# Optimization experiments

Measured on AMD Instinct MI355X. Metric: run time of the kernel, lower is better.

The kernel has to match this reference:

```python
import jax, jax.numpy as jnp
import numpy as np
import math

EMBED = 1024
HEADS = 16
HEAD_DIM = EMBED // HEADS
FFN = 4 * EMBED
LAYERS = 3
SEQ = 2048
BATCH = 2
INPUT_DIM = 64


def make_pe(max_len, d_model):
    pe = np.zeros((max_len, d_model), dtype=np.float32)
    pos = np.arange(max_len, dtype=np.float32)[:, None]
    div = np.exp(np.arange(0, d_model, 2, dtype=np.float32) * (-math.log(10000.0) / d_model))
    pe[:, 0::2] = np.sin(pos * div)
    pe[:, 1::2] = np.cos(pos * div)
    return jnp.asarray(pe)


def setup_inputs() -> dict:
    key = jax.random.key(0)
    ks = jax.random.split(key, 16)
    s = lambda k, shape, fan: jax.random.normal(k, shape, dtype=jnp.float32) / np.sqrt(fan)
    return {
        "x": jax.random.normal(ks[0], (BATCH, SEQ, INPUT_DIM), dtype=jnp.float32),
        "mask": jnp.ones((BATCH, 1, 1, SEQ), dtype=bool),
        "embed_W": s(ks[1], (INPUT_DIM, EMBED), INPUT_DIM),
        "embed_b": jnp.zeros((EMBED,), jnp.float32),
        "pe": make_pe(SEQ, EMBED),
        "Wq": s(ks[2], (LAYERS, HEAD_DIM, HEAD_DIM), HEAD_DIM),
        "Wk": s(ks[3], (LAYERS, HEAD_DIM, HEAD_DIM), HEAD_DIM),
        "Wv": s(ks[4], (LAYERS, HEAD_DIM, HEAD_DIM), HEAD_DIM),
        "Wo": s(ks[5], (LAYERS, EMBED, EMBED), EMBED),
        "bo": jnp.zeros((LAYERS, EMBED), jnp.float32),
        "ln1_g": jnp.ones((LAYERS, EMBED), jnp.float32),
        "ln1_b": jnp.zeros((LAYERS, EMBED), jnp.float32),
        "W1": s(ks[6], (LAYERS, EMBED, FFN), EMBED),
        "b1": jnp.zeros((LAYERS, FFN), jnp.float32),
        "W2": s(ks[7], (LAYERS, FFN, EMBED), FFN),
        "b2": jnp.zeros((LAYERS, EMBED), jnp.float32),
        "ln2_g": jnp.ones((LAYERS, EMBED), jnp.float32),
        "ln2_b": jnp.zeros((LAYERS, EMBED), jnp.float32),
    }


def _layernorm(x, g, b, eps=1e-5):
    mu = jnp.mean(x, axis=-1, keepdims=True)
    var = jnp.var(x, axis=-1, keepdims=True)
    return (x - mu) * jax.lax.rsqrt(var + eps) * g + b


def reference(x, mask, embed_W, embed_b, pe, Wq, Wk, Wv, Wo, bo,
              ln1_g, ln1_b, W1, b1, W2, b2, ln2_g, ln2_b):
    N, S, _ = x.shape
    scale = 1.0 / np.sqrt(EMBED).astype(np.float32)  # note: sqrt(embed_size), as in original
    h = x @ embed_W + embed_b + pe[None, :S, :]
    for l in range(LAYERS):
        hr = h.reshape(N, S, HEADS, HEAD_DIM)
        q = jnp.einsum('nshd,de->nshe', hr, Wq[l])
        k = jnp.einsum('nshd,de->nshe', hr, Wk[l])
        v = jnp.einsum('nshd,de->nshe', hr, Wv[l])
        energy = jnp.einsum('nqhd,nkhd->nhqk', q, k)  # (N,H,S,S)
        energy = jnp.where(mask == 0, jnp.float32(-1e20), energy)
        attn = jax.nn.softmax(energy * scale, axis=-1)
        o = jnp.einsum('nhqk,nkhd->nqhd', attn, v).reshape(N, S, EMBED)
        o = o @ Wo[l] + bo[l]
        x1 = _layernorm(o + h, ln1_g[l], ln1_b[l])
        ff = jax.nn.relu(x1 @ W1[l] + b1[l]) @ W2[l] + b2[l]
        h = _layernorm(ff + x1, ln2_g[l], ln2_b[l])
    return h
```

## Files before the change

### kernel.cpp

```cpp
#include <hip/hip_runtime.h>


typedef __attribute__((ext_vector_type(8))) unsigned short us8;
typedef __attribute__((ext_vector_type(4))) unsigned short us4;
typedef __attribute__((ext_vector_type(8))) __bf16 bf16x8;
typedef __attribute__((ext_vector_type(4))) float f32x4;

#define SEQ   2048
#define HEADS 16
#define HD    64
#define EMB   1024
#define FFN_  4096
#define NBAT  2
#define ROWS  (NBAT*SEQ)

__device__ __forceinline__ float bf2f(unsigned short s) {
    return __builtin_bit_cast(float, ((unsigned int)s) << 16);
}
__device__ __forceinline__ unsigned short f2bf(float f) {
    unsigned int u = __builtin_bit_cast(unsigned int, f);
    u += 0x7fffu + ((u >> 16) & 1u);
    return (unsigned short)(u >> 16);
}
__device__ __forceinline__ bf16x8 ldfrag(const unsigned short* p) {
    us8 v = *(const us8*)p;
    return __builtin_bit_cast(bf16x8, v);
}
__device__ __forceinline__ us8 cvt8(const float* p) {
    float4 f0 = *(const float4*)p, f1 = *(const float4*)(p + 4);
    us8 v;
    v[0] = f2bf(f0.x); v[1] = f2bf(f0.y); v[2] = f2bf(f0.z); v[3] = f2bf(f0.w);
    v[4] = f2bf(f1.x); v[5] = f2bf(f1.y); v[6] = f2bf(f1.z); v[7] = f2bf(f1.w);
    return v;
}
__device__ __forceinline__ void async_cp16(const unsigned short* g, unsigned short* l) {
    __builtin_amdgcn_global_load_lds(
        (const __attribute__((address_space(1))) void*)g,
        (__attribute__((address_space(3))) void*)l, 16, 0, 0);
}

__device__ __forceinline__ void transpose_tile(
    const float* __restrict__ W, unsigned short* __restrict__ Wt,
    int K, int N, int k0, int n0, int t)
{
    __shared__ float T[64][65];
    const int kk = t >> 4, nn = (t & 15) * 4;
#pragma unroll
    for (int r = 0; r < 4; r++) {
        float4 v = *(const float4*)(W + (size_t)(k0 + kk + r*16)*N + n0 + nn);
        T[kk + r*16][nn+0] = v.x; T[kk + r*16][nn+1] = v.y;
        T[kk + r*16][nn+2] = v.z; T[kk + r*16][nn+3] = v.w;
    }
    __syncthreads();
    const int n = t >> 2, kc = (t & 3) * 16;
    us8 a, b;
#pragma unroll
    for (int i = 0; i < 8; i++) a[i] = f2bf(T[kc + i][n]);
#pragma unroll
    for (int i = 0; i < 8; i++) b[i] = f2bf(T[kc + 8 + i][n]);
    *(us8*)(Wt + (size_t)(n0 + n)*K + k0 + kc)     = a;
    *(us8*)(Wt + (size_t)(n0 + n)*K + k0 + kc + 8) = b;
}

__global__ __launch_bounds__(256) void wprep(
    const float* __restrict__ W, unsigned short* __restrict__ Wt,
    const int K, const int N)
{
    transpose_tile(W, Wt, K, N, blockIdx.x*64, blockIdx.y*64, threadIdx.x);
}

__global__ __launch_bounds__(256) void wprep_qkv(
    const float* __restrict__ Wq, const float* __restrict__ Wk,
    const float* __restrict__ Wv, unsigned short* __restrict__ Wt3)
{
    const float* W = blockIdx.z == 0 ? Wq : (blockIdx.z == 1 ? Wk : Wv);
    transpose_tile(W, Wt3 + (size_t)blockIdx.z*64*64, 64, 64, 0, 0, threadIdx.x);
}

__global__ __launch_bounds__(256) void cvt_bf16(
    const float* __restrict__ src, unsigned short* __restrict__ dst, const int n8)
{
    int i = blockIdx.x*256 + threadIdx.x;
    if (i < n8) *(us8*)(dst + (size_t)i*8) = cvt8(src + (size_t)i*8);
}

__global__ __launch_bounds__(256) void vtrans(
    const unsigned short* __restrict__ QKV, unsigned short* __restrict__ Vt)
{
    __shared__ __align__(16) unsigned short T[64*72];
    const int s0 = blockIdx.x*64, h = blockIdx.y, n = blockIdx.z;
    const int t = threadIdx.x;
    const int s = t & 63, c16 = (t >> 6) * 16;
    const unsigned short* src =
        QKV + ((size_t)(n*SEQ + s0 + s)*HEADS + h)*192 + 128 + c16;
    *(us8*)&T[s*72 + c16]     = *(const us8*)(src);
    *(us8*)&T[s*72 + c16 + 8] = *(const us8*)(src + 8);
    __syncthreads();
    const int f = t & 63, r16 = (t >> 6) * 16;
    us8 a, b;
#pragma unroll
    for (int i = 0; i < 8; i++) a[i] = T[(r16 + i)*72 + f];
#pragma unroll
    for (int i = 0; i < 8; i++) b[i] = T[(r16 + 8 + i)*72 + f];
    unsigned short* dst = Vt + ((size_t)(n*HEADS + h)*HD + f)*SEQ + s0 + r16;
    *(us8*)dst       = a;
    *(us8*)(dst + 8) = b;
}

template<int BM, int BN, int WR, int WC>
__global__ __launch_bounds__(WR*WC*64) void gemm_bt(
    const unsigned short* __restrict__ A, const unsigned short* __restrict__ Bt,
    void* __restrict__ Cout, const int out_bf16,
    const float* __restrict__ bias, const float* __restrict__ pe,
    const int M, const int N, const int K, const int relu)
{
    constexpr int BK  = 32;
    constexpr int NW  = WR*WC;
    constexpr int ACH = BM*4;
    constexpr int BCH = BN*4;
    constexpr int APW = ACH/NW;
    constexpr int BPW = BCH/NW;
    __shared__ __align__(16) unsigned short As[BM*BK];
    __shared__ __align__(16) unsigned short Bs[BN*BK];

    const int tid  = threadIdx.x;
    const int lane = tid & 63;
    const int wave = tid >> 6;
    const int wm   = (wave / WC) * 64;
    const int wn   = (wave % WC) * 64;
    const int bm   = blockIdx.x * BM;
    const int bn   = blockIdx.y * BN;
    const int m15  = lane & 15;
    const int quad = lane >> 4;

    f32x4 acc[4][4];
#pragma unroll
    for (int i = 0; i < 4; i++)
#pragma unroll
        for (int j = 0; j < 4; j++) acc[i][j] = (f32x4){0.f, 0.f, 0.f, 0.f};

    for (int kt = 0; kt < K; kt += BK) {
#pragma unroll
        for (int j = 0; j < APW/64; j++) {
            const int c = wave*APW + j*64 + lane;
            async_cp16(A + (size_t)(bm + (c >> 2))*K + kt + (c & 3)*8,
                       As + (size_t)(wave*APW + j*64)*8);
        }
#pragma unroll
        for (int j = 0; j < BPW/64; j++) {
            const int c = wave*BPW + j*64 + lane;
            async_cp16(Bt + (size_t)(bn + (c >> 2))*K + kt + (c & 3)*8,
                       Bs + (size_t)(wave*BPW + j*64)*8);
        }
        __syncthreads();

        bf16x8 af[4], bfr[4];
#pragma unroll
        for (int i = 0; i < 4; i++) af[i]  = ldfrag(&As[(wm + i*16 + m15)*BK + quad*8]);
#pragma unroll
        for (int j = 0; j < 4; j++) bfr[j] = ldfrag(&Bs[(wn + j*16 + m15)*BK + quad*8]);
#pragma unroll
        for (int i = 0; i < 4; i++)
#pragma unroll
            for (int j = 0; j < 4; j++)
                acc[i][j] = __builtin_amdgcn_mfma_f32_16x16x32_bf16(af[i], bfr[j], acc[i][j], 0, 0, 0);
        __syncthreads();
    }

#pragma unroll
    for (int i = 0; i < 4; i++) {
#pragma unroll
        for (int j = 0; j < 4; j++) {
#pragma unroll
            for (int r = 0; r < 4; r++) {
                int row = bm + wm + i*16 + quad*4 + r;
                int col = bn + wn + j*16 + m15;
                float v = acc[i][j][r];
                if (bias) v += bias[col];
                if (pe)   v += pe[(size_t)(row & (SEQ-1))*EMB + col];
                if (relu) v = fmaxf(v, 0.f);
                if (out_bf16) ((unsigned short*)Cout)[(size_t)row*N + col] = f2bf(v);
                else          ((float*)Cout)[(size_t)row*N + col] = v;
            }
        }
    }
}

__global__ __launch_bounds__(256, 2) void flash_attn(
    const unsigned short* __restrict__ QKV, const unsigned short* __restrict__ Vt,
    unsigned short* __restrict__ O)
{
    const int h = blockIdx.y, n = blockIdx.z;
    const int tid = threadIdx.x, lane = tid & 63, wave = tid >> 6;
    const int m15 = lane & 15, quad = lane >> 4;
    const int q0 = blockIdx.x*128 + wave*32;

    __shared__ __align__(16) unsigned short Pl[4][32*36];

    bf16x8 aq[2][2];
#pragma unroll
    for (int mi = 0; mi < 2; mi++) {
        const unsigned short* qp =
            QKV + ((size_t)(n*SEQ + q0 + mi*16 + m15)*HEADS + h)*192;
        aq[mi][0] = ldfrag(qp + quad*8);
        aq[mi][1] = ldfrag(qp + 32 + quad*8);
    }

    f32x4 accO[2][4];
    f32x4 lacc[2];
#pragma unroll
    for (int mi = 0; mi < 2; mi++) {
        lacc[mi] = (f32x4){0.f, 0.f, 0.f, 0.f};
#pragma unroll
        for (int ft = 0; ft < 4; ft++) accO[mi][ft] = (f32x4){0.f, 0.f, 0.f, 0.f};
    }

    const float sl2e = 0.03125f * 1.4426950408889634f;
    const unsigned short* kb = QKV + ((size_t)(n*SEQ)*HEADS + h)*192 + 64;
    const unsigned short* vb = Vt + (size_t)(n*HEADS + h)*HD*SEQ;

    us8 ones_u;
#pragma unroll
    for (int i = 0; i < 8; i++) ones_u[i] = 0x3F80;
    const bf16x8 ones = __builtin_bit_cast(bf16x8, ones_u);

    auto load_kv = [&](bf16x8 (&dk)[2][2], bf16x8 (&dv)[4], int kt) {
#pragma unroll
        for (int nt = 0; nt < 2; nt++)
#pragma unroll
            for (int ks = 0; ks < 2; ks++)
                dk[nt][ks] = ldfrag(kb + (size_t)(kt + nt*16 + m15)*(HEADS*192)
                                       + ks*32 + quad*8);
#pragma unroll
        for (int ft = 0; ft < 4; ft++)
            dv[ft] = ldfrag(vb + (size_t)(ft*16 + m15)*SEQ + kt + quad*8);
    };

    auto step = [&](bf16x8 (&ck)[2][2], bf16x8 (&cv)[4],
                    bf16x8 (&nk)[2][2], bf16x8 (&nv)[4], int ktn) {
        load_kv(nk, nv, ktn);
        __builtin_amdgcn_sched_barrier(0);

        f32x4 sv[2][2];
        __builtin_amdgcn_s_setprio(1);
#pragma unroll
        for (int mi = 0; mi < 2; mi++)
#pragma unroll
            for (int nt = 0; nt < 2; nt++) {
                f32x4 z = (f32x4){0.f, 0.f, 0.f, 0.f};
                z = __builtin_amdgcn_mfma_f32_16x16x32_bf16(aq[mi][0], ck[nt][0], z, 0, 0, 0);
                z = __builtin_amdgcn_mfma_f32_16x16x32_bf16(aq[mi][1], ck[nt][1], z, 0, 0, 0);
                sv[mi][nt] = z;
            }
        __builtin_amdgcn_s_setprio(0);

#pragma unroll
        for (int mi = 0; mi < 2; mi++)
#pragma unroll
            for (int nt = 0; nt < 2; nt++)
#pragma unroll
                for (int r = 0; r < 4; r++) {
                    float p = exp2f(fminf(sv[mi][nt][r] * sl2e, 80.f));
                    Pl[wave][(mi*16 + quad*4 + r)*36 + nt*16 + m15] = f2bf(p);
                }

        bf16x8 pf[2];
#pragma unroll
        for (int mi = 0; mi < 2; mi++)
            pf[mi] = ldfrag(&Pl[wave][(mi*16 + m15)*36 + quad*8]);
        __builtin_amdgcn_s_setprio(1);
#pragma unroll
        for (int mi = 0; mi < 2; mi++) {
#pragma unroll
            for (int ft = 0; ft < 4; ft++)
                accO[mi][ft] = __builtin_amdgcn_mfma_f32_16x16x32_bf16(
                    pf[mi], cv[ft], accO[mi][ft], 0, 0, 0);
            lacc[mi] = __builtin_amdgcn_mfma_f32_16x16x32_bf16(
                pf[mi], ones, lacc[mi], 0, 0, 0);
        }
        __builtin_amdgcn_s_setprio(0);
    };

    bf16x8 k0[2][2], v0[4], k1[2][2], v1[4];
    load_kv(k0, v0, 0);
    for (int kt = 0; kt < SEQ; kt += 64) {
        step(k0, v0, k1, v1, kt + 32);
        step(k1, v1, k0, v0, (kt + 64) & (SEQ - 1));
    }

#pragma unroll
    for (int mi = 0; mi < 2; mi++)
#pragma unroll
        for (int r = 0; r < 4; r++) {
            const float inv = 1.0f / lacc[mi][r];
            const int row = q0 + mi*16 + quad*4 + r;
#pragma unroll
            for (int ft = 0; ft < 4; ft++)
                O[((size_t)(n*SEQ + row)*HEADS + h)*HD + ft*16 + m15] =
                    f2bf(accO[mi][ft][r] * inv);
        }
}

__global__ __launch_bounds__(256) void add_ln_kernel(
    const unsigned short* __restrict__ a, const unsigned short* __restrict__ res,
    const float* __restrict__ g, const float* __restrict__ b,
    void* __restrict__ out, const int out_fp32)
{
    const int row = blockIdx.x;
    const int tid = threadIdx.x;
    const int c0  = tid * 4;

    us4 va = *(const us4*)(a   + (size_t)row*EMB + c0);
    us4 vr = *(const us4*)(res + (size_t)row*EMB + c0);
    float x[4];
#pragma unroll
    for (int i = 0; i < 4; i++) x[i] = bf2f(va[i]) + bf2f(vr[i]);

    float s = x[0] + x[1] + x[2] + x[3];
    float q = x[0]*x[0] + x[1]*x[1] + x[2]*x[2] + x[3]*x[3];
#pragma unroll
    for (int off = 1; off < 64; off <<= 1) {
        s += __shfl_xor(s, off, 64);
        q += __shfl_xor(q, off, 64);
    }
    __shared__ float rs[4], rq[4];
    if ((tid & 63) == 0) { rs[tid >> 6] = s; rq[tid >> 6] = q; }
    __syncthreads();
    s = rs[0] + rs[1] + rs[2] + rs[3];
    q = rq[0] + rq[1] + rq[2] + rq[3];

    const float mu   = s * (1.0f/EMB);
    const float var  = q * (1.0f/EMB) - mu*mu;
    const float rstd = rsqrtf(var + 1e-5f);

    float4 vg = *(const float4*)(g + c0);
    float4 vb = *(const float4*)(b + c0);
    float y0 = (x[0] - mu) * rstd * vg.x + vb.x;
    float y1 = (x[1] - mu) * rstd * vg.y + vb.y;
    float y2 = (x[2] - mu) * rstd * vg.z + vb.z;
    float y3 = (x[3] - mu) * rstd * vg.w + vb.w;

    if (out_fp32) {
        *(float4*)((float*)out + (size_t)row*EMB + c0) = (float4){y0, y1, y2, y3};
    } else {
        us4 o;
        o[0] = f2bf(y0); o[1] = f2bf(y1); o[2] = f2bf(y2); o[3] = f2bf(y3);
        *(us4*)((unsigned short*)out + (size_t)row*EMB + c0) = o;
    }
}

extern "C" void kernel_launch(void* const* d_in, const int* in_sizes, int n_in,
                              void* d_out, int out_size, void* d_ws, size_t ws_size,
                              hipStream_t stream)
{
    (void)in_sizes; (void)n_in; (void)out_size; (void)ws_size;
    const float* x    = (const float*)d_in[0];
    const float* embW = (const float*)d_in[2];
    const float* embB = (const float*)d_in[3];
    const float* pe   = (const float*)d_in[4];
    const float* Wq   = (const float*)d_in[5];
    const float* Wk   = (const float*)d_in[6];
    const float* Wv   = (const float*)d_in[7];
    const float* Wo   = (const float*)d_in[8];
    const float* bo   = (const float*)d_in[9];
    const float* ln1g = (const float*)d_in[10];
    const float* ln1b = (const float*)d_in[11];
    const float* W1   = (const float*)d_in[12];
    const float* b1   = (const float*)d_in[13];
    const float* W2   = (const float*)d_in[14];
    const float* b2   = (const float*)d_in[15];
    const float* ln2g = (const float*)d_in[16];
    const float* ln2b = (const float*)d_in[17];

    char* ws = (char*)d_ws;
    const size_t MB = 1024*1024;
    unsigned short* qkv = (unsigned short*)ws;
    unsigned short* ff  = (unsigned short*)ws;
    unsigned short* vt  = (unsigned short*)(ws + 24*MB);
    unsigned short* t   = (unsigned short*)(ws + 32*MB);
    unsigned short* h   = (unsigned short*)(ws + 40*MB);
    unsigned short* x1  = (unsigned short*)(ws + 48*MB);
    unsigned short* wx  = (unsigned short*)(ws + 56*MB);
    unsigned short* xb    = t;
    unsigned short* embWt = t + 256*1024;
    unsigned short* qkvWt = t;
    unsigned short* o   = (unsigned short*)d_out;

    cvt_bf16<<<128, 256, 0, stream>>>(x, xb, ROWS*64/8);
    wprep<<<dim3(1, EMB/64), 256, 0, stream>>>(embW, embWt, 64, EMB);
    gemm_bt<128,128,2,2><<<dim3(ROWS/128, EMB/128), 256, 0, stream>>>(
        xb, embWt, h, 1, embB, pe, ROWS, EMB, 64, 0);

    for (int l = 0; l < 3; l++) {
        wprep_qkv<<<dim3(1,1,3), 256, 0, stream>>>(
            Wq + (size_t)l*HD*HD, Wk + (size_t)l*HD*HD, Wv + (size_t)l*HD*HD, qkvWt);
        gemm_bt<256,64,4,1><<<dim3(ROWS*HEADS/256, 3), 256, 0, stream>>>(
            h, qkvWt, qkv, 1, nullptr, nullptr, ROWS*HEADS, 192, HD, 0);

        vtrans<<<dim3(SEQ/64, HEADS, NBAT), 256, 0, stream>>>(qkv, vt);
        flash_attn<<<dim3(SEQ/128, HEADS, NBAT), 256, 0, stream>>>(qkv, vt, o);

        wprep<<<dim3(EMB/64, EMB/64), 256, 0, stream>>>(
            Wo + (size_t)l*EMB*EMB, wx, EMB, EMB);
        gemm_bt<128,128,2,2><<<dim3(ROWS/128, EMB/128), 256, 0, stream>>>(
            o, wx, t, 1, bo + (size_t)l*EMB, nullptr, ROWS, EMB, EMB, 0);
        add_ln_kernel<<<ROWS, 256, 0, stream>>>(
            t, h, ln1g + (size_t)l*EMB, ln1b + (size_t)l*EMB, x1, 0);

        wprep<<<dim3(EMB/64, FFN_/64), 256, 0, stream>>>(
            W1 + (size_t)l*EMB*FFN_, wx, EMB, FFN_);
        gemm_bt<128,128,2,2><<<dim3(ROWS/128, FFN_/128), 256, 0, stream>>>(
            x1, wx, ff, 1, b1 + (size_t)l*FFN_, nullptr, ROWS, FFN_, EMB, 1);
        wprep<<<dim3(FFN_/64, EMB/64), 256, 0, stream>>>(
            W2 + (size_t)l*FFN_*EMB, wx, FFN_, EMB);
        gemm_bt<128,128,2,2><<<dim3(ROWS/128, EMB/128), 256, 0, stream>>>(
            ff, wx, t, 1, b2 + (size_t)l*EMB, nullptr, ROWS, EMB, FFN_, 0);

        if (l == 2)
            add_ln_kernel<<<ROWS, 256, 0, stream>>>(
                t, x1, ln2g + (size_t)l*EMB, ln2b + (size_t)l*EMB, d_out, 1);
        else
            add_ln_kernel<<<ROWS, 256, 0, stream>>>(
                t, x1, ln2g + (size_t)l*EMB, ln2b + (size_t)l*EMB, h, 0);
    }
}
```

Measured before the change: 1.336 ms.

## Split flash attention key range across two wave groups with LDS reduction

Doubles the attention block to 512 threads, with two groups of four waves each processing half of the key sequence for the same query tile. Partial output accumulators and row sums from the second group are exchanged through shared memory and added into the first group's results before normalization and store. This aims to raise parallelism and latency hiding per query tile. In exchange it adds a shared-memory reduction, two barriers, and more register and LDS pressure per block, which can limit occupancy. The split is only valid because softmax here uses no running max, so partial sums add directly.

```diff
diff --git a/kernel.cpp b/kernel.cpp
--- a/kernel.cpp
+++ b/kernel.cpp
@@ -186,16 +186,22 @@
     }
 }
 
-__global__ __launch_bounds__(256, 2) void flash_attn(
+#define HALF (SEQ/2)
+
+__global__ __launch_bounds__(512, 2) void flash_attn(
     const unsigned short* __restrict__ QKV, const unsigned short* __restrict__ Vt,
     unsigned short* __restrict__ O)
 {
     const int h = blockIdx.y, n = blockIdx.z;
     const int tid = threadIdx.x, lane = tid & 63, wave = tid >> 6;
+    const int W4 = wave & 3, grp = wave >> 2;
     const int m15 = lane & 15, quad = lane >> 4;
-    const int q0 = blockIdx.x*128 + wave*32;
-
-    __shared__ __align__(16) unsigned short Pl[4][32*36];
+    const int q0 = blockIdx.x*128 + W4*32;
+    const int base = grp * HALF;
+
+    __shared__ __align__(16) char smbuf[4*40*64*4];
+    unsigned short (*Pl)[32*36] = (unsigned short (*)[32*36])smbuf;
+    float (*ex)[40][64]         = (float (*)[40][64])smbuf;
 
     bf16x8 aq[2][2];
 #pragma unroll
@@ -282,23 +288,54 @@
     };
 
     bf16x8 k0[2][2], v0[4], k1[2][2], v1[4];
-    load_kv(k0, v0, 0);
-    for (int kt = 0; kt < SEQ; kt += 64) {
+    load_kv(k0, v0, base);
+    for (int kt = base; kt < base + HALF; kt += 64) {
         step(k0, v0, k1, v1, kt + 32);
-        step(k1, v1, k0, v0, (kt + 64) & (SEQ - 1));
-    }
-
-#pragma unroll
-    for (int mi = 0; mi < 2; mi++)
-#pragma unroll
-        for (int r = 0; r < 4; r++) {
-            const float inv = 1.0f / lacc[mi][r];
-            const int row = q0 + mi*16 + quad*4 + r;
+        step(k1, v1, k0, v0, base + ((kt + 64 - base) & (HALF - 1)));
+    }
+
+    __syncthreads();
+    if (grp == 1) {
+#pragma unroll
+        for (int mi = 0; mi < 2; mi++)
 #pragma unroll
             for (int ft = 0; ft < 4; ft++)
-                O[((size_t)(n*SEQ + row)*HEADS + h)*HD + ft*16 + m15] =
-                    f2bf(accO[mi][ft][r] * inv);
-        }
+#pragma unroll
+                for (int r = 0; r < 4; r++)
+                    ex[W4][mi*16 + ft*4 + r][lane] = accO[mi][ft][r];
+#pragma unroll
+        for (int mi = 0; mi < 2; mi++)
+#pragma unroll
+            for (int r = 0; r < 4; r++)
+                ex[W4][32 + mi*4 + r][lane] = lacc[mi][r];
+    }
+    __syncthreads();
+    if (grp == 0) {
+#pragma unroll
+        for (int mi = 0; mi < 2; mi++)
+#pragma unroll
+            for (int ft = 0; ft < 4; ft++)
+#pragma unroll
+                for (int r = 0; r < 4; r++)
+                    accO[mi][ft][r] += ex[W4][mi*16 + ft*4 + r][lane];
+#pragma unroll
+        for (int mi = 0; mi < 2; mi++)
+#pragma unroll
+            for (int r = 0; r < 4; r++)
+                lacc[mi][r] += ex[W4][32 + mi*4 + r][lane];
+
+#pragma unroll
+        for (int mi = 0; mi < 2; mi++)
+#pragma unroll
+            for (int r = 0; r < 4; r++) {
+                const float inv = 1.0f / lacc[mi][r];
+                const int row = q0 + mi*16 + quad*4 + r;
+#pragma unroll
+                for (int ft = 0; ft < 4; ft++)
+                    O[((size_t)(n*SEQ + row)*HEADS + h)*HD + ft*16 + m15] =
+                        f2bf(accO[mi][ft][r] * inv);
+            }
+    }
 }
 
 __global__ __launch_bounds__(256) void add_ln_kernel(
@@ -398,7 +435,7 @@
             h, qkvWt, qkv, 1, nullptr, nullptr, ROWS*HEADS, 192, HD, 0);
 
         vtrans<<<dim3(SEQ/64, HEADS, NBAT), 256, 0, stream>>>(qkv, vt);
-        flash_attn<<<dim3(SEQ/128, HEADS, NBAT), 256, 0, stream>>>(qkv, vt, o);
+        flash_attn<<<dim3(SEQ/128, HEADS, NBAT), 512, 0, stream>>>(qkv, vt, o);
 
         wprep<<<dim3(EMB/64, EMB/64), 256, 0, stream>>>(
             Wo + (size_t)l*EMB*EMB, wx, EMB, EMB);
```

Measured after the change: 1.343 ms. No clear change (+0.6%).
